# Kernel optimization log

Hardware: AMD Instinct MI355X
Metric: run time of the kernel (lower is better)

The kernel has to match this reference:

```python
import jax, jax.numpy as jnp
import numpy as np

N_NODES = 500000
D = 128          # input_dim
UNITS = 128
K = 32           # neigh_max
B = 20000        # batch of target nodes
LEAKY_ALPHA = 0.2  # tf.nn.leaky_relu default


def setup_inputs() -> dict:
    key = jax.random.key(0)
    k1, k2, k3, k4, k5, k6, k7 = jax.random.split(key, 7)
    features = jax.random.normal(k1, (N_NODES, D), dtype=jnp.float32)
    node = jax.random.randint(k2, (B, 1), 0, N_NODES, dtype=jnp.int32)
    neighbours = jax.random.randint(k3, (B, K), 0, N_NODES, dtype=jnp.int32)
    # learned parameters (glorot-scale random)
    kernel = jax.random.normal(k4, (1, D, D), dtype=jnp.float32) * (1.0 / np.sqrt(D))
    kernel1 = jax.random.normal(k5, (1, D, D), dtype=jnp.float32) * (1.0 / np.sqrt(D))
    attention_weights = jax.random.normal(k6, (1, 2 * D), dtype=jnp.float32) * (1.0 / np.sqrt(2 * D))
    neigh_weights = jax.random.normal(k7, (D, UNITS), dtype=jnp.float32) * (1.0 / np.sqrt(D))
    return {
        "features": features,
        "node": node,
        "neighbours": neighbours,
        "kernel": kernel,
        "kernel1": kernel1,
        "attention_weights": attention_weights,
        "neigh_weights": neigh_weights,
    }


def reference(features, node, neighbours, kernel, kernel1, attention_weights, neigh_weights):
    # gather: node_feat [B,1,D], neigh_feat [B,K,D]
    node_feat = features[node]
    neigh_feat = features[neighbours]
    # per-node projections (kernel tiled over batch in original == shared matmul)
    node_h = jnp.einsum('bkd,de->bke', node_feat, kernel[0])    # [B,1,D]
    neigh_h = jnp.einsum('bkd,de->bke', neigh_feat, kernel1[0])  # [B,K,D]
    # concat [neigh, tiled node] -> [B,K,2D]
    tile_node = jnp.broadcast_to(node_h, neigh_h.shape)
    concat_feat = jnp.concatenate([neigh_h, tile_node], axis=2)
    # attention score: [B,K,2D] @ [2D,1] -> [B,K,1], leaky_relu (alpha=0.2)
    score = concat_feat @ attention_weights.reshape(2 * D, 1)
    score = jnp.where(score > 0, score, LEAKY_ALPHA * score)
    # softmax over neighbors (axis K)
    final_score = jax.nn.softmax(score, axis=1)                  # [B,K,1]
    # weighted aggregate: neigh_h^T @ score -> [B,D]
    attention_feat = jnp.einsum('bkd,bk->bd', neigh_h, final_score[..., 0])
    # output projection
    return attention_feat @ neigh_weights                        # [B,UNITS]
```

## Files before the change

kernel.cpp:

```cpp
#include <hip/hip_runtime.h>
#include <hip/hip_bf16.h>

#define D 128
#define K 32
#define NB 20000
#define NPB 4
#define NBLK (NB / NPB)
#define NROWS 33
#define FSTR 64

typedef unsigned short u16;
typedef unsigned int   u32;

__device__ inline float blo(u32 v) { return __uint_as_float(v << 16); }
__device__ inline float bhi(u32 v) { return __uint_as_float(v & 0xffff0000u); }
__device__ inline u32 f2b_rne(float x) {
    u32 u = __float_as_uint(x);
    return (u + 0x7fffu + ((u >> 16) & 1u)) >> 16;
}
__device__ inline u32 pack2(float a, float b) { return f2b_rne(a) | (f2b_rne(b) << 16); }

__global__ __launch_bounds__(256)
void precompute_kernel(const float* __restrict__ k0, const float* __restrict__ k1,
                       const float* __restrict__ aw, const float* __restrict__ nw,
                       float* __restrict__ w12, u16* __restrict__ MTb)
{
    int t = threadIdx.x;
    if (blockIdx.x < 64) {
        int gid = blockIdx.x * 256 + t;
        int u = gid & 127, d = gid >> 7;
        float acc = 0.f;
        #pragma unroll 8
        for (int e = 0; e < D; ++e)
            acc = fmaf(k1[d * D + e], nw[e * D + u], acc);
        MTb[u * D + d] = (u16)f2b_rne(acc);
    } else {
        if (t < 128) {
            float acc = 0.f;
            #pragma unroll 8
            for (int e = 0; e < D; ++e)
                acc = fmaf(k1[t * D + e], aw[e], acc);
            w12[t] = acc;
        } else {
            int d = t - 128;
            float acc = 0.f;
            #pragma unroll 8
            for (int e = 0; e < D; ++e)
                acc = fmaf(k0[d * D + e], aw[128 + e], acc);
            w12[t] = acc;
        }
    }
}

__global__ __launch_bounds__(256, 4)
void gat4_kernel(const float* __restrict__ features,
                 const int* __restrict__ node,
                 const int* __restrict__ neigh,
                 const float* __restrict__ w12g,
                 const u16* __restrict__ MTb,
                 float* __restrict__ out)
{
    __shared__ u32 fbuf[128 * FSTR];

    const int t  = threadIdx.x;
    const int b4 = blockIdx.x * NPB;
    const int n  = t >> 6;
    const int l  = t & 63;
    const int cc = l & 31;
    const int h  = l >> 5;

    const float4* w4 = (const float4*)w12g;
    const float4 wlo = w4[cc];
    const float4 whi = w4[32 + cc];

    const int idxv = neigh[(b4 + n) * K + cc];
    const int tidx = node[b4 + n];

    const float4* f4 = (const float4*)features;

    float4 v0[8], v1[8], vt;
    #pragma unroll
    for (int i = 0; i < 8; ++i)
        v0[i] = f4[(size_t)__shfl(idxv, 2 * i + h) * 32 + cc];
    if (h == 0) vt = f4[(size_t)tidx * 32 + cc];

    float sc = 0.f, sct = 0.f;

    #pragma unroll
    for (int i = 0; i < 8; ++i) {
        v1[i] = f4[(size_t)__shfl(idxv, 2 * (i + 8) + h) * 32 + cc];
        const int r = 4 * (2 * i + h) + n;
        u32* dst = &fbuf[r * FSTR + cc * 2];
        dst[0] = pack2(v0[i].x, v0[i].y);
        dst[1] = pack2(v0[i].z, v0[i].w);
        float p = v0[i].x * wlo.x + v0[i].y * wlo.y + v0[i].z * wlo.z + v0[i].w * wlo.w;
        p += __shfl_xor(p, 1);
        p += __shfl_xor(p, 2);
        p += __shfl_xor(p, 4);
        p += __shfl_xor(p, 8);
        p += __shfl_xor(p, 16);
        if ((cc >> 1) == i) sc = p;
    }

    if (h == 0) {
        float p = vt.x * whi.x + vt.y * whi.y + vt.z * whi.z + vt.w * whi.w;
        p += __shfl_xor(p, 1);
        p += __shfl_xor(p, 2);
        p += __shfl_xor(p, 4);
        p += __shfl_xor(p, 8);
        p += __shfl_xor(p, 16);
        sct = p;
    }

    #pragma unroll
    for (int i = 0; i < 8; ++i) {
        const int k = 2 * (i + 8) + h;
        const int r = 4 * k + n;
        u32* dst = &fbuf[r * FSTR + cc * 2];
        dst[0] = pack2(v1[i].x, v1[i].y);
        dst[1] = pack2(v1[i].z, v1[i].w);
        float p = v1[i].x * wlo.x + v1[i].y * wlo.y + v1[i].z * wlo.z + v1[i].w * wlo.w;
        p += __shfl_xor(p, 1);
        p += __shfl_xor(p, 2);
        p += __shfl_xor(p, 4);
        p += __shfl_xor(p, 8);
        p += __shfl_xor(p, 16);
        if ((cc >> 1) == i + 8) sc = p;
    }

    float vsc = __shfl(sc, ((cc & 1) << 5) | cc);
    vsc += __shfl(sct, 0);
    vsc = vsc > 0.f ? vsc : 0.2f * vsc;
    float m = vsc;
    m = fmaxf(m, __shfl_xor(m, 1));
    m = fmaxf(m, __shfl_xor(m, 2));
    m = fmaxf(m, __shfl_xor(m, 4));
    m = fmaxf(m, __shfl_xor(m, 8));
    m = fmaxf(m, __shfl_xor(m, 16));
    float e = __expf(vsc - m);
    float s = e;
    s += __shfl_xor(s, 1);
    s += __shfl_xor(s, 2);
    s += __shfl_xor(s, 4);
    s += __shfl_xor(s, 8);
    s += __shfl_xor(s, 16);
    const float a = e * (1.0f / s);

    float a0 = 0.f, a1 = 0.f;
    #pragma unroll
    for (int k = 0; k < K; ++k) {
        float al = __shfl(a, k);
        u32 vv = fbuf[(4 * k + n) * FSTR + l];
        a0 = fmaf(al, blo(vv), a0);
        a1 = fmaf(al, bhi(vv), a1);
    }

    const uint4* mrowA = (const uint4*)(MTb + (size_t)l * D);
    const uint4* mrowB = (const uint4*)(MTb + (size_t)(l + 64) * D);
    float accA = 0.f, accB = 0.f;
    #pragma unroll
    for (int q = 0; q < 16; ++q) {
        float g0 = __shfl(a0, 4 * q + 0), g1 = __shfl(a1, 4 * q + 0);
        float g2 = __shfl(a0, 4 * q + 1), g3 = __shfl(a1, 4 * q + 1);
        float g4 = __shfl(a0, 4 * q + 2), g5 = __shfl(a1, 4 * q + 2);
        float g6 = __shfl(a0, 4 * q + 3), g7 = __shfl(a1, 4 * q + 3);
        uint4 x = mrowA[q], y = mrowB[q];
        accA += g0 * blo(x.x) + g1 * bhi(x.x) + g2 * blo(x.y) + g3 * bhi(x.y)
              + g4 * blo(x.z) + g5 * bhi(x.z) + g6 * blo(x.w) + g7 * bhi(x.w);
        accB += g0 * blo(y.x) + g1 * bhi(y.x) + g2 * blo(y.y) + g3 * bhi(y.y)
              + g4 * blo(y.z) + g5 * bhi(y.z) + g6 * blo(y.w) + g7 * bhi(y.w);
    }
    out[(size_t)(b4 + n) * D + l]      = accA;
    out[(size_t)(b4 + n) * D + 64 + l] = accB;
}

#define RS 33
#define RSF 132
__global__ __launch_bounds__(256)
void gat_fallback_kernel(const float* __restrict__ features, const int* __restrict__ node,
                         const int* __restrict__ neigh,
                         const float* __restrict__ k0, const float* __restrict__ k1,
                         const float* __restrict__ aw, const float* __restrict__ nw,
                         float* __restrict__ out)
{
    __shared__ float4 fbuf[NROWS * RS];
    __shared__ float w1[D], w2[D], h[D];
    __shared__ int   idxs[NROWS];
    __shared__ float psum[NROWS][8];
    __shared__ float zb[NROWS], alpha[K], agg[D];

    const int b = blockIdx.x, t = threadIdx.x;

    if (t < 128) {
        float a = 0.f;
        for (int e = 0; e < D; ++e) a = fmaf(k1[t * D + e], aw[e], a);
        w1[t] = a;
    } else {
        int d = t - 128;
        float a = 0.f;
        for (int e = 0; e < D; ++e) a = fmaf(k0[d * D + e], aw[128 + e], a);
        w2[d] = a;
    }
    if (t < K)       idxs[t] = neigh[b * K + t];
    else if (t == K) idxs[K] = node[b];
    __syncthreads();

    const float4* f4 = (const float4*)features;
    for (int c = t; c < NROWS * 32; c += 256) {
        int j = c >> 5, cc = c & 31;
        fbuf[j * RS + cc] = f4[(size_t)idxs[j] * 32 + cc];
    }
    __syncthreads();

    for (int task = t; task < NROWS * 8; task += 256) {
        int j = task >> 3, sub = task & 7;
        const float* w = (j < K) ? w1 : w2;
        const float4* r = &fbuf[j * RS + sub * 4];
        int d0 = sub * 16;
        float4 a0 = r[0], a1 = r[1], a2 = r[2], a3 = r[3];
        float acc;
        acc  = a0.x * w[d0 + 0]  + a0.y * w[d0 + 1]  + a0.z * w[d0 + 2]  + a0.w * w[d0 + 3];
        acc += a1.x * w[d0 + 4]  + a1.y * w[d0 + 5]  + a1.z * w[d0 + 6]  + a1.w * w[d0 + 7];
        acc += a2.x * w[d0 + 8]  + a2.y * w[d0 + 9]  + a2.z * w[d0 + 10] + a2.w * w[d0 + 11];
        acc += a3.x * w[d0 + 12] + a3.y * w[d0 + 13] + a3.z * w[d0 + 14] + a3.w * w[d0 + 15];
        psum[j][sub] = acc;
    }
    __syncthreads();

    if (t < NROWS) {
        float s = 0.f;
        #pragma unroll
        for (int i = 0; i < 8; ++i) s += psum[t][i];
        zb[t] = s;
    }
    __syncthreads();

    if (t == 0) {
        float c = zb[K];
        float m = -1e30f;
        #pragma unroll
        for (int k = 0; k < K; ++k) {
            float v = zb[k] + c;
            v = v > 0.f ? v : 0.2f * v;
            zb[k] = v;
            m = fmaxf(m, v);
        }
        float s = 0.f;
        #pragma unroll
        for (int k = 0; k < K; ++k) { float e = __expf(zb[k] - m); alpha[k] = e; s += e; }
        float inv = 1.f / s;
        #pragma unroll
        for (int k = 0; k < K; ++k) alpha[k] *= inv;
    }
    __syncthreads();

    const float* fb = (const float*)fbuf;
    if (t < D) {
        float a = 0.f;
        #pragma unroll
        for (int k = 0; k < K; ++k)
            a = fmaf(alpha[k], fb[k * RSF + t], a);
        agg[t] = a;
    }
    __syncthreads();

    if (t < 128) {
        float acc = 0.f;
        for (int d = 0; d < D; ++d) acc = fmaf(agg[d], k1[d * D + t], acc);
        h[t] = acc;
    }
    __syncthreads();
    if (t < 128) {
        float acc = 0.f;
        for (int e = 0; e < D; ++e) acc = fmaf(h[e], nw[e * D + t], acc);
        out[(size_t)b * D + t] = acc;
    }
}

extern "C" void kernel_launch(void* const* d_in, const int* in_sizes, int n_in,
                              void* d_out, int out_size, void* d_ws, size_t ws_size,
                              hipStream_t stream) {
    const float* features = (const float*)d_in[0];
    const int*   node     = (const int*)d_in[1];
    const int*   neigh    = (const int*)d_in[2];
    const float* k0       = (const float*)d_in[3];
    const float* k1       = (const float*)d_in[4];
    const float* aw       = (const float*)d_in[5];
    const float* nw       = (const float*)d_in[6];

    const size_t need = 256 * sizeof(float) + (size_t)D * D * sizeof(u16);
    if (ws_size >= need) {
        float* w12 = (float*)d_ws;
        u16*   MTb = (u16*)(w12 + 256);
        precompute_kernel<<<65, 256, 0, stream>>>(k0, k1, aw, nw, w12, MTb);
        gat4_kernel<<<NBLK, 256, 0, stream>>>(features, node, neigh, w12, MTb,
                                              (float*)d_out);
    } else {
        gat_fallback_kernel<<<NB, 256, 0, stream>>>(features, node, neigh,
                                                    k0, k1, aw, nw, (float*)d_out);
    }
}
```

Baseline: 428.9 us.

## Issue all 16 neighbour loads up front, use hardware bf16 packing

Result: no change. 424.8 us (-1.0%).

```diff
diff --git a/kernel.cpp b/kernel.cpp
--- a/kernel.cpp
+++ b/kernel.cpp
@@ -18,7 +18,12 @@
     u32 u = __float_as_uint(x);
     return (u + 0x7fffu + ((u >> 16) & 1u)) >> 16;
 }
-__device__ inline u32 pack2(float a, float b) { return f2b_rne(a) | (f2b_rne(b) << 16); }
+__device__ inline u32 packcvt(float a, float b) {
+    __hip_bfloat162 h = __float22bfloat162_rn(make_float2(a, b));
+    union { __hip_bfloat162 h2; u32 u; } cv;
+    cv.h2 = h;
+    return cv.u;
+}
 
 __global__ __launch_bounds__(256)
 void precompute_kernel(const float* __restrict__ k0, const float* __restrict__ k1,
@@ -52,7 +57,7 @@
     }
 }
 
-__global__ __launch_bounds__(256, 4)
+__global__ __launch_bounds__(256)
 void gat4_kernel(const float* __restrict__ features,
                  const int* __restrict__ node,
                  const int* __restrict__ neigh,
@@ -78,22 +83,22 @@
 
     const float4* f4 = (const float4*)features;
 
-    float4 v0[8], v1[8], vt;
-    #pragma unroll
-    for (int i = 0; i < 8; ++i)
-        v0[i] = f4[(size_t)__shfl(idxv, 2 * i + h) * 32 + cc];
+    float4 v[16], vt;
+    #pragma unroll
+    for (int i = 0; i < 16; ++i)
+        v[i] = f4[(size_t)__shfl(idxv, 2 * i + h) * 32 + cc];
     if (h == 0) vt = f4[(size_t)tidx * 32 + cc];
 
+    __builtin_amdgcn_sched_barrier(0);
+
     float sc = 0.f, sct = 0.f;
-
-    #pragma unroll
-    for (int i = 0; i < 8; ++i) {
-        v1[i] = f4[(size_t)__shfl(idxv, 2 * (i + 8) + h) * 32 + cc];
-        const int r = 4 * (2 * i + h) + n;
-        u32* dst = &fbuf[r * FSTR + cc * 2];
-        dst[0] = pack2(v0[i].x, v0[i].y);
-        dst[1] = pack2(v0[i].z, v0[i].w);
-        float p = v0[i].x * wlo.x + v0[i].y * wlo.y + v0[i].z * wlo.z + v0[i].w * wlo.w;
+    #pragma unroll
+    for (int i = 0; i < 16; ++i) {
+        const int k = 2 * i + h;
+        u32* dst = &fbuf[(n * 32 + k) * FSTR + cc * 2];
+        dst[0] = packcvt(v[i].x, v[i].y);
+        dst[1] = packcvt(v[i].z, v[i].w);
+        float p = v[i].x * wlo.x + v[i].y * wlo.y + v[i].z * wlo.z + v[i].w * wlo.w;
         p += __shfl_xor(p, 1);
         p += __shfl_xor(p, 2);
         p += __shfl_xor(p, 4);
@@ -101,7 +106,6 @@
         p += __shfl_xor(p, 16);
         if ((cc >> 1) == i) sc = p;
     }
-
     if (h == 0) {
         float p = vt.x * whi.x + vt.y * whi.y + vt.z * whi.z + vt.w * whi.w;
         p += __shfl_xor(p, 1);
@@ -110,22 +114,6 @@
         p += __shfl_xor(p, 8);
         p += __shfl_xor(p, 16);
         sct = p;
-    }
-
-    #pragma unroll
-    for (int i = 0; i < 8; ++i) {
-        const int k = 2 * (i + 8) + h;
-        const int r = 4 * k + n;
-        u32* dst = &fbuf[r * FSTR + cc * 2];
-        dst[0] = pack2(v1[i].x, v1[i].y);
-        dst[1] = pack2(v1[i].z, v1[i].w);
-        float p = v1[i].x * wlo.x + v1[i].y * wlo.y + v1[i].z * wlo.z + v1[i].w * wlo.w;
-        p += __shfl_xor(p, 1);
-        p += __shfl_xor(p, 2);
-        p += __shfl_xor(p, 4);
-        p += __shfl_xor(p, 8);
-        p += __shfl_xor(p, 16);
-        if ((cc >> 1) == i + 8) sc = p;
     }
 
     float vsc = __shfl(sc, ((cc & 1) << 5) | cc);
@@ -150,7 +138,7 @@
     #pragma unroll
     for (int k = 0; k < K; ++k) {
         float al = __shfl(a, k);
-        u32 vv = fbuf[(4 * k + n) * FSTR + l];
+        u32 vv = fbuf[(n * 32 + k) * FSTR + l];
         a0 = fmaf(al, blo(vv), a0);
         a1 = fmaf(al, bhi(vv), a1);
     }
```
